# Kernel optimization log

Hardware: AMD Instinct MI355X
Metric: run time of the kernel (lower is better)

## Reference

```python
import jax, jax.numpy as jnp
import numpy as np

KNOTS = 16
BOUND = 5.0
BN_EPS = 1e-5


def _rq_spline_fwd(x, W, H, D, B):
    # x: (N, d); W, H: (N, d, K) bin widths/heights summing to 2B; D: (N, d, K-1) internal derivatives
    N, d = x.shape
    K = W.shape[-1]
    pad_lo = jnp.full((N, d, 1), -B, dtype=x.dtype)
    xk = jnp.concatenate([pad_lo, -B + jnp.cumsum(W, axis=-1)], axis=-1)  # (N,d,K+1) knot x positions
    yk = jnp.concatenate([pad_lo, -B + jnp.cumsum(H, axis=-1)], axis=-1)  # (N,d,K+1) knot y positions
    dk = jnp.pad(D, ((0, 0), (0, 0), (1, 1)), constant_values=1.0)        # (N,d,K+1) derivs, boundaries = 1

    oob = (x <= -B) | (x >= B)
    xs = jnp.where(oob, 0.0, x)  # safe in-range value for bin search/eval

    # per-element bin search: index of bin containing xs
    idx = jnp.clip(jnp.sum(xs[..., None] >= xk[..., :-1], axis=-1) - 1, 0, K - 1)  # (N,d)

    take = lambda a: jnp.take_along_axis(a, idx[..., None], axis=-1)[..., 0]
    wk = take(W)
    hk = take(H)
    xk0 = take(xk[..., :-1])
    yk0 = take(yk[..., :-1])
    d0 = take(dk[..., :-1])
    d1 = take(dk[..., 1:])
    sk = hk / wk

    t = (xs - xk0) / wk            # relative position in bin, in [0,1]
    omt = 1.0 - t
    num = hk * (sk * t * t + d0 * t * omt)
    den = sk + (d1 + d0 - 2.0 * sk) * t * omt
    y = yk0 + num / den
    ld = jnp.log(sk * sk * (d1 * t * t + 2.0 * sk * t * omt + d0 * omt * omt)) - 2.0 * jnp.log(den)

    y = jnp.where(oob, x, y)
    ld = jnp.where(oob, 0.0, ld)
    return y, jnp.sum(ld, axis=-1)


def setup_inputs() -> dict:
    key = jax.random.key(0)
    ks = jax.random.split(key, 6)
    N, Dm, K = 262144, 16, 8
    H1, H2 = 128, 128
    ds = Dm // 2
    spline_dim = 3 * KNOTS - 1  # 47
    f32 = jnp.float32
    return {
        "x": jax.random.normal(ks[0], (N, Dm), dtype=f32),
        "c": jax.random.normal(ks[1], (N, K), dtype=f32),
        "bn_scale": jnp.ones((ds + K,), f32),
        "bn_bias": jnp.zeros((ds + K,), f32),
        "bn_mean": jnp.zeros((ds + K,), f32),
        "bn_var": jnp.ones((ds + K,), f32),
        "W1": jax.random.normal(ks[2], (ds + K, H1), dtype=f32) * (1.0 / np.sqrt(ds + K)),
        "b1": jnp.zeros((H1,), f32),
        "W2": jax.random.normal(ks[3], (H1, H2), dtype=f32) * (1.0 / np.sqrt(H1)),
        "b2": jnp.zeros((H2,), f32),
        "W3": jax.random.normal(ks[4], (H2, ds * spline_dim), dtype=f32) * (1.0 / np.sqrt(H2)),
        "b3": jnp.zeros((ds * spline_dim,), f32),
    }


def reference(x, c, bn_scale, bn_bias, bn_mean, bn_var, W1, b1, W2, b2, W3, b3):
    N, Dm = x.shape
    ds = Dm // 2
    lower, upper = x[:, :ds], x[:, ds:]

    h = jnp.hstack([upper, c])
    # BatchNorm with running stats (train=False)
    h = (h - bn_mean) * jax.lax.rsqrt(bn_var + BN_EPS) * bn_scale + bn_bias
    h = jax.nn.swish(h @ W1 + b1)
    h = jax.nn.swish(h @ W2 + b2)
    h = (h @ W3 + b3).reshape(N, ds, 3 * KNOTS - 1)

    dx = 2.0 * BOUND * jax.nn.softmax(h[..., :KNOTS], axis=-1)
    dy = 2.0 * BOUND * jax.nn.softmax(h[..., KNOTS:2 * KNOTS], axis=-1)
    sl = jax.nn.softplus(h[..., 2 * KNOTS:])

    y_low, log_det = _rq_spline_fwd(lower, dx, dy, sl, BOUND)
    y = jnp.hstack([y_low, upper])
    return y, log_det
```

## Files before the change

kernel.cpp:

```cpp
#include <hip/hip_runtime.h>
#include <math.h>

#define NTHREADS 512
#define BR 64
#define H3W 390

typedef __attribute__((ext_vector_type(8))) short short8;
typedef __attribute__((ext_vector_type(4))) float f32x4;

#define W1OFF 0
#define W2OFF 4096
#define W3OFF 20480
#define WCH   69632

__device__ __forceinline__ unsigned short f2bf(float f) {
    unsigned u = __float_as_uint(f);
    u += 0x7fffu + ((u >> 16) & 1u);
    return (unsigned short)(u >> 16);
}
__device__ __forceinline__ float bf2f(unsigned short h) {
    return __uint_as_float(((unsigned)h) << 16);
}
__device__ __forceinline__ float frcp(float x) { return __builtin_amdgcn_rcpf(x); }
__device__ __forceinline__ void split2(float v, unsigned short& hi, unsigned short& lo) {
    unsigned u = __float_as_uint(v);
    hi = (unsigned short)(u >> 16);
    float lof = v - __uint_as_float(u & 0xFFFF0000u);
    lo = (unsigned short)(__float_as_uint(lof) >> 16);
}

__global__ void pack_weights(const float* __restrict__ W1, const float* __restrict__ W2,
                             const float* __restrict__ W3,
                             const float* __restrict__ bn_scale, const float* __restrict__ bn_bias,
                             const float* __restrict__ bn_mean, const float* __restrict__ bn_var,
                             const float* __restrict__ b1,
                             unsigned short* __restrict__ ws) {
    int idx = blockIdx.x * blockDim.x + threadIdx.x;
    if (idx >= 69760) return;
    if (idx >= 69632) {
        int n = idx - 69632;
        float acc = b1[n];
        for (int k = 0; k < 16; ++k) {
            float s = bn_scale[k] * rsqrtf(bn_var[k] + 1e-5f);
            float t = bn_bias[k] - bn_mean[k] * s;
            acc += t * W1[k * 128 + n];
        }
        ((float*)(ws + 2 * WCH))[n] = acc;
        return;
    }
    int k, n, tileIdx, base;
    float v;
    if (idx < 4096) {
        k = idx >> 7; n = idx & 127;
        if (k < 16) {
            float s = bn_scale[k] * rsqrtf(bn_var[k] + 1e-5f);
            v = s * W1[k * 128 + n];
        } else v = 0.0f;
        base = W1OFF; tileIdx = (n >> 4);
    } else if (idx < 20480) {
        int j = idx - 4096; k = j >> 7; n = j & 127;
        v = W2[k * 128 + n];
        base = W2OFF; tileIdx = (k >> 5) * 8 + (n >> 4);
    } else {
        int j = idx - 20480; k = j / 384; n = j - k * 384;
        v = (n < 376) ? W3[k * 376 + n] : 0.0f;
        base = W3OFF; tileIdx = (k >> 5) * 24 + (n >> 4);
    }
    int dst = base + tileIdx * 512 + ((k & 31) >> 3) * 128 + (n & 15) * 8 + (k & 7);
    unsigned short hi = f2bf(v);
    unsigned short lo = f2bf(v - bf2f(hi));
    ws[dst]       = hi;
    ws[dst + WCH] = lo;
}

__device__ __forceinline__ short8 ldsA(const unsigned short* h, int mt, int kt, int lane) {
    int row  = mt * 16 + (lane & 15);
    int byte = row * 256 + kt * 64 + ((lane >> 4) << 4);
    byte ^= (row & 7) << 4;
    return *reinterpret_cast<const short8*>(reinterpret_cast<const char*>(h) + byte);
}
__device__ __forceinline__ short8 ldsA0(const unsigned short* h, int mt, int lane) {
    int row  = mt * 16 + (lane & 15);
    int byte = row * 80 + ((lane >> 4) << 4);
    return *reinterpret_cast<const short8*>(reinterpret_cast<const char*>(h) + byte);
}
__device__ __forceinline__ short8 ldB(const unsigned short* w, int tileIdx, int lane) {
    return *reinterpret_cast<const short8*>(w + (tileIdx * 64 + lane) * 8);
}
__device__ __forceinline__ void stH(unsigned short* h, int row, int col, unsigned short v) {
    int byte = row * 256 + col * 2;
    byte ^= (row & 7) << 4;
    *reinterpret_cast<unsigned short*>(reinterpret_cast<char*>(h) + byte) = v;
}

__global__ __launch_bounds__(NTHREADS, 2)
void nsc_mfma(const float* __restrict__ x, const float* __restrict__ c,
              const float* __restrict__ b2, const float* __restrict__ b3,
              const unsigned short* __restrict__ wpk,
              float* __restrict__ out, int N)
{
    __shared__ __align__(16) char smem[65536];
    unsigned short* h1hi = (unsigned short*)(smem);
    unsigned short* h1lo = (unsigned short*)(smem + 16384);
    unsigned short* h2hi = (unsigned short*)(smem + 32768);
    unsigned short* h2lo = (unsigned short*)(smem + 49152);
    unsigned short* h0hi = (unsigned short*)(smem + 32768);
    unsigned short* h0lo = (unsigned short*)(smem + 37888);
    _Float16*       h3   = (_Float16*)(smem);

    const unsigned short* wlo = wpk + WCH;
    const float* b1p = (const float*)(wpk + 2 * WCH);

    const int tid  = threadIdx.x;
    const int lane = tid & 63;
    const int wv   = tid >> 6;
    const int row0 = blockIdx.x * BR;

    for (int i = tid; i < BR * 16; i += NTHREADS) {
        const int r = i >> 4, col = i & 15;
        int row = row0 + r; if (row >= N) row = N - 1;
        float v = (col < 8) ? x[row * 16 + 8 + col] : c[row * 8 + (col - 8)];
        unsigned short hi, lo; split2(v, hi, lo);
        h0hi[r * 40 + col] = hi;      h0lo[r * 40 + col] = lo;
        h0hi[r * 40 + 16 + col] = 0;  h0lo[r * 40 + 16 + col] = 0;
    }
    __syncthreads();

    {
        f32x4 acc[4];
        #pragma unroll
        for (int m = 0; m < 4; ++m) acc[m] = (f32x4){0.f, 0.f, 0.f, 0.f};
        short8 bhi = ldB(wpk + W1OFF, wv, lane);
        short8 blo = ldB(wlo + W1OFF, wv, lane);
        #pragma unroll
        for (int m = 0; m < 4; ++m) {
            short8 ahi = ldsA0(h0hi, m, lane);
            short8 alo = ldsA0(h0lo, m, lane);
            acc[m] = __builtin_amdgcn_mfma_f32_16x16x32_bf16(alo, bhi, acc[m], 0, 0, 0);
            acc[m] = __builtin_amdgcn_mfma_f32_16x16x32_bf16(ahi, blo, acc[m], 0, 0, 0);
            acc[m] = __builtin_amdgcn_mfma_f32_16x16x32_bf16(ahi, bhi, acc[m], 0, 0, 0);
        }
        const int col = wv * 16 + (lane & 15);
        const float bias = b1p[col];
        #pragma unroll
        for (int m = 0; m < 4; ++m) {
            #pragma unroll
            for (int r = 0; r < 4; ++r) {
                const int row = m * 16 + (lane >> 4) * 4 + r;
                float v = acc[m][r] + bias;
                v = v * frcp(1.0f + __expf(-v));
                unsigned short hi, lo; split2(v, hi, lo);
                stH(h1hi, row, col, hi);
                stH(h1lo, row, col, lo);
            }
        }
    }
    __syncthreads();

    {
        f32x4 acc[4];
        #pragma unroll
        for (int m = 0; m < 4; ++m) acc[m] = (f32x4){0.f, 0.f, 0.f, 0.f};
        #pragma unroll
        for (int kt = 0; kt < 4; ++kt) {
            short8 bhi = ldB(wpk + W2OFF, kt * 8 + wv, lane);
            short8 blo = ldB(wlo + W2OFF, kt * 8 + wv, lane);
            #pragma unroll
            for (int m = 0; m < 4; ++m) {
                short8 ahi = ldsA(h1hi, m, kt, lane);
                short8 alo = ldsA(h1lo, m, kt, lane);
                acc[m] = __builtin_amdgcn_mfma_f32_16x16x32_bf16(alo, bhi, acc[m], 0, 0, 0);
                acc[m] = __builtin_amdgcn_mfma_f32_16x16x32_bf16(ahi, blo, acc[m], 0, 0, 0);
                acc[m] = __builtin_amdgcn_mfma_f32_16x16x32_bf16(ahi, bhi, acc[m], 0, 0, 0);
            }
        }
        const int col = wv * 16 + (lane & 15);
        const float bias = b2[col];
        #pragma unroll
        for (int m = 0; m < 4; ++m) {
            #pragma unroll
            for (int r = 0; r < 4; ++r) {
                const int row = m * 16 + (lane >> 4) * 4 + r;
                float v = acc[m][r] + bias;
                v = v * frcp(1.0f + __expf(-v));
                unsigned short hi, lo; split2(v, hi, lo);
                stH(h2hi, row, col, hi);
                stH(h2lo, row, col, lo);
            }
        }
    }
    __syncthreads();

    {
        const int nt0 = wv * 3;
        f32x4 acc[4][3];
        #pragma unroll
        for (int m = 0; m < 4; ++m)
            #pragma unroll
            for (int i = 0; i < 3; ++i) acc[m][i] = (f32x4){0.f, 0.f, 0.f, 0.f};
        #pragma unroll
        for (int kt = 0; kt < 4; ++kt) {
            short8 ahi[4], alo[4];
            #pragma unroll
            for (int m = 0; m < 4; ++m) { ahi[m] = ldsA(h2hi, m, kt, lane); alo[m] = ldsA(h2lo, m, kt, lane); }
            #pragma unroll
            for (int i = 0; i < 3; ++i) {
                const int t = kt * 24 + nt0 + i;
                short8 bhi = ldB(wpk + W3OFF, t, lane);
                short8 blo = ldB(wlo + W3OFF, t, lane);
                #pragma unroll
                for (int m = 0; m < 4; ++m) {
                    acc[m][i] = __builtin_amdgcn_mfma_f32_16x16x32_bf16(alo[m], bhi, acc[m][i], 0, 0, 0);
                    acc[m][i] = __builtin_amdgcn_mfma_f32_16x16x32_bf16(ahi[m], blo, acc[m][i], 0, 0, 0);
                    acc[m][i] = __builtin_amdgcn_mfma_f32_16x16x32_bf16(ahi[m], bhi, acc[m][i], 0, 0, 0);
                }
            }
        }
        __syncthreads();
        #pragma unroll
        for (int i = 0; i < 3; ++i) {
            const int col = (nt0 + i) * 16 + (lane & 15);
            const float bias = (col < 376) ? b3[col] : 0.0f;
            #pragma unroll
            for (int m = 0; m < 4; ++m) {
                #pragma unroll
                for (int r = 0; r < 4; ++r) {
                    const int row = m * 16 + (lane >> 4) * 4 + r;
                    h3[row * H3W + col] = (_Float16)(acc[m][i][r] + bias);
                }
            }
        }
    }
    __syncthreads();

    const int r   = tid >> 3;
    const int dd  = tid & 7;
    const int row = row0 + r;

    float acc[47];
    #pragma unroll
    for (int j = 0; j < 47; ++j) acc[j] = (float)h3[r * H3W + dd * 47 + j];

    float m = -INFINITY;
    #pragma unroll
    for (int j = 0; j < 16; ++j) m = fmaxf(m, acc[j]);
    float eW[16]; float sW = 0.0f;
    #pragma unroll
    for (int j = 0; j < 16; ++j) { eW[j] = __expf(acc[j] - m); sW += eW[j]; }

    m = -INFINITY;
    #pragma unroll
    for (int j = 0; j < 16; ++j) m = fmaxf(m, acc[16 + j]);
    float eH[16]; float sH = 0.0f;
    #pragma unroll
    for (int j = 0; j < 16; ++j) { eH[j] = __expf(acc[16 + j] - m); sH += eH[j]; }

    const float x0  = x[row * 16 + dd];
    const bool oob  = (x0 <= -5.0f) || (x0 >= 5.0f);
    const float xs  = oob ? 0.0f : x0;

    const float u = (xs + 5.0f) * (sW * 0.1f);
    float cum = 0.0f, ycum = 0.0f;
    float selx = 0.0f, sely = 0.0f;
    float wke = eW[0], hke = eH[0];
    float d0r = 0.0f, d1r = acc[32];
    bool d0one = true, d1one = false;
    #pragma unroll
    for (int k = 1; k < 16; ++k) {
        cum  += eW[k - 1];
        ycum += eH[k - 1];
        if (u >= cum) {
            selx = cum; sely = ycum;
            wke = eW[k]; hke = eH[k];
            d0r = acc[31 + k]; d0one = false;
            d1r = (k < 15) ? acc[32 + k] : 0.0f;
            d1one = (k == 15);
        }
    }
    const float d0 = d0one ? 1.0f : (fmaxf(d0r, 0.0f) + __logf(1.0f + __expf(-fabsf(d0r))));
    const float d1 = d1one ? 1.0f : (fmaxf(d1r, 0.0f) + __logf(1.0f + __expf(-fabsf(d1r))));

    const float invW = 10.0f * frcp(sW);
    const float invH = 10.0f * frcp(sH);
    const float xk0 = -5.0f + invW * selx;
    const float yk0 = -5.0f + invH * sely;
    const float wk  = invW * wke;
    const float hk  = invH * hke;

    const float rwk = frcp(wk);
    const float sk  = hk * rwk;
    const float t   = (xs - xk0) * rwk;
    const float omt = 1.0f - t;
    const float num = hk * (sk * t * t + d0 * t * omt);
    const float den = sk + (d1 + d0 - 2.0f * sk) * t * omt;
    const float rden = frcp(den);
    float y  = yk0 + num * rden;
    float ld = __logf(sk * sk * (d1 * t * t + 2.0f * sk * t * omt + d0 * omt * omt) * rden * rden);
    if (oob) { y = x0; ld = 0.0f; }

    ld += __shfl_xor(ld, 1);
    ld += __shfl_xor(ld, 2);
    ld += __shfl_xor(ld, 4);

    if (row < N) {
        out[row * 16 + dd]     = y;
        out[row * 16 + 8 + dd] = x[row * 16 + 8 + dd];
        if (dd == 0) out[N * 16 + row] = ld;
    }
}

extern "C" void kernel_launch(void* const* d_in, const int* in_sizes, int n_in,
                              void* d_out, int out_size, void* d_ws, size_t ws_size,
                              hipStream_t stream) {
    const float* x        = (const float*)d_in[0];
    const float* c        = (const float*)d_in[1];
    const float* bn_scale = (const float*)d_in[2];
    const float* bn_bias  = (const float*)d_in[3];
    const float* bn_mean  = (const float*)d_in[4];
    const float* bn_var   = (const float*)d_in[5];
    const float* W1       = (const float*)d_in[6];
    const float* b1       = (const float*)d_in[7];
    const float* W2       = (const float*)d_in[8];
    const float* b2       = (const float*)d_in[9];
    const float* W3       = (const float*)d_in[10];
    const float* b3       = (const float*)d_in[11];
    float* out            = (float*)d_out;
    unsigned short* wpk   = (unsigned short*)d_ws;

    const int N = in_sizes[0] / 16;

    pack_weights<<<273, 256, 0, stream>>>(W1, W2, W3, bn_scale, bn_bias, bn_mean, bn_var,
                                          b1, wpk);

    const int grid = (N + BR - 1) / BR;
    nsc_mfma<<<grid, NTHREADS, 0, stream>>>(x, c, b2, b3, wpk, out, N);
}
```

Before: 133.9 us.

## Pad W3 columns per dimension to 48 and vectorize swizzled h3 LDS reads

Repacks W3 and b3 so each spline dimension's 47 outputs occupy a 48-wide, 16-byte aligned slot, with the bias pre-padded in the workspace. The h3 tile in LDS is stored with a 768-byte row stride and an XOR swizzle. Each thread then reads its 47 values as six 16-byte vector loads instead of 47 scalar half loads. This targets LDS instruction count and bank conflicts in the spline epilogue, at the cost of a slightly larger pack kernel and extra index arithmetic.

Measured after the change: 127.0 us. 1.05x faster.

```diff
diff --git a/kernel.cpp b/kernel.cpp
--- a/kernel.cpp
+++ b/kernel.cpp
@@ -3,7 +3,6 @@
 
 #define NTHREADS 512
 #define BR 64
-#define H3W 390
 
 typedef __attribute__((ext_vector_type(8))) short short8;
 typedef __attribute__((ext_vector_type(4))) float f32x4;
@@ -33,10 +32,16 @@
                              const float* __restrict__ W3,
                              const float* __restrict__ bn_scale, const float* __restrict__ bn_bias,
                              const float* __restrict__ bn_mean, const float* __restrict__ bn_var,
-                             const float* __restrict__ b1,
+                             const float* __restrict__ b1, const float* __restrict__ b3,
                              unsigned short* __restrict__ ws) {
     int idx = blockIdx.x * blockDim.x + threadIdx.x;
-    if (idx >= 69760) return;
+    if (idx >= 70144) return;
+    if (idx >= 69760) {
+        int n = idx - 69760;
+        int j = n & 47;
+        ((float*)(ws + 2 * WCH))[128 + n] = (j < 47) ? b3[(n >> 4) / 3 * 47 + j] : 0.0f;
+        return;
+    }
     if (idx >= 69632) {
         int n = idx - 69632;
         float acc = b1[n];
@@ -63,7 +68,8 @@
         base = W2OFF; tileIdx = (k >> 5) * 8 + (n >> 4);
     } else {
         int j = idx - 20480; k = j / 384; n = j - k * 384;
-        v = (n < 376) ? W3[k * 376 + n] : 0.0f;
+        int jj = n % 48, dd = n / 48;
+        v = (jj < 47) ? W3[k * 376 + dd * 47 + jj] : 0.0f;
         base = W3OFF; tileIdx = (k >> 5) * 24 + (n >> 4);
     }
     int dst = base + tileIdx * 512 + ((k & 31) >> 3) * 128 + (n & 15) * 8 + (k & 7);
@@ -95,7 +101,7 @@
 
 __global__ __launch_bounds__(NTHREADS, 2)
 void nsc_mfma(const float* __restrict__ x, const float* __restrict__ c,
-              const float* __restrict__ b2, const float* __restrict__ b3,
+              const float* __restrict__ b2,
               const unsigned short* __restrict__ wpk,
               float* __restrict__ out, int N)
 {
@@ -106,10 +112,10 @@
     unsigned short* h2lo = (unsigned short*)(smem + 49152);
     unsigned short* h0hi = (unsigned short*)(smem + 32768);
     unsigned short* h0lo = (unsigned short*)(smem + 37888);
-    _Float16*       h3   = (_Float16*)(smem);
 
     const unsigned short* wlo = wpk + WCH;
     const float* b1p = (const float*)(wpk + 2 * WCH);
+    const float* b3p = b1p + 128;
 
     const int tid  = threadIdx.x;
     const int lane = tid & 63;
@@ -220,13 +226,14 @@
         #pragma unroll
         for (int i = 0; i < 3; ++i) {
             const int col = (nt0 + i) * 16 + (lane & 15);
-            const float bias = (col < 376) ? b3[col] : 0.0f;
+            const float bias = b3p[col];
             #pragma unroll
             for (int m = 0; m < 4; ++m) {
                 #pragma unroll
                 for (int r = 0; r < 4; ++r) {
                     const int row = m * 16 + (lane >> 4) * 4 + r;
-                    h3[row * H3W + col] = (_Float16)(acc[m][i][r] + bias);
+                    int byte = (row * 768 + col * 2) ^ ((row & 7) << 4);
+                    *(_Float16*)(smem + byte) = (_Float16)(acc[m][i][r] + bias);
                 }
             }
         }
@@ -236,10 +243,16 @@
     const int r   = tid >> 3;
     const int dd  = tid & 7;
     const int row = row0 + r;
-
+    const int swz = (r & 7) << 4;
+
+    short8 ch[6];
+    #pragma unroll
+    for (int j16 = 0; j16 < 6; ++j16)
+        ch[j16] = *reinterpret_cast<const short8*>(smem + ((r * 768 + dd * 96 + j16 * 16) ^ swz));
     float acc[47];
     #pragma unroll
-    for (int j = 0; j < 47; ++j) acc[j] = (float)h3[r * H3W + dd * 47 + j];
+    for (int j = 0; j < 47; ++j)
+        acc[j] = (float)(((const _Float16*)&ch[j >> 3])[j & 7]);
 
     float m = -INFINITY;
     #pragma unroll
@@ -329,9 +342,9 @@
 
     const int N = in_sizes[0] / 16;
 
-    pack_weights<<<273, 256, 0, stream>>>(W1, W2, W3, bn_scale, bn_bias, bn_mean, bn_var,
-                                          b1, wpk);
+    pack_weights<<<274, 256, 0, stream>>>(W1, W2, W3, bn_scale, bn_bias, bn_mean, bn_var,
+                                          b1, b3, wpk);
 
     const int grid = (N + BR - 1) / BR;
-    nsc_mfma<<<grid, NTHREADS, 0, stream>>>(x, c, b2, b3, wpk, out, N);
-}
+    nsc_mfma<<<grid, NTHREADS, 0, stream>>>(x, c, b2, wpk, out, N);
+}
```
